# Kernel tuning notes

Measured on AMD Instinct MI355X. Metric: run time of the kernel, lower is better.

The kernel has to match this reference:

```python
import jax, jax.numpy as jnp
import numpy as np

N = 100000   # nodes
D = 8        # in_dim/2 (per-node phase dim)
H = 256      # hidden_dim
E = 1600000  # directed edges (avg degree 16)


def setup_inputs() -> dict:
    key = jax.random.key(0)
    ks = jax.random.split(key, 8)
    q = jax.random.normal(ks[0], (N, D), jnp.float32)
    p = jax.random.normal(ks[1], (N, D), jnp.float32)
    # per-node diagonal positive-definite mass matrix (what get_mass() produces:
    # diag(relu(diag(.)) + 1e-4)); keep it well-conditioned for the inverse.
    m_diag = jax.random.uniform(ks[2], (N, D), jnp.float32) + 0.5
    M = jax.vmap(jnp.diag)(m_diag)  # [N, D, D]
    src = jax.random.randint(ks[3], (E,), 0, N, dtype=jnp.int32)
    off = jax.random.randint(ks[4], (E,), 1, N, dtype=jnp.int32)
    dst = ((src + off) % N).astype(jnp.int32)  # guaranteed no self-edges (euclid>0)
    W1 = jax.random.normal(ks[5], (D, H), jnp.float32) / jnp.sqrt(D)
    b1 = jnp.zeros((H,), jnp.float32)
    W2 = jax.random.normal(ks[6], (H, D), jnp.float32) / jnp.sqrt(H)
    b2 = jnp.zeros((D,), jnp.float32)
    gravity = jnp.ones((1, 1), jnp.float32)
    return {"q": q, "p": p, "M": M, "src": src, "dst": dst,
            "W1": W1, "b1": b1, "W2": W2, "b2": b2, "gravity": gravity}


def _gcn(x, src, dst, norm_src, norm_dst, W, b, n_nodes):
    # DGL GraphConv norm='both': D_out^{-1/2} on src, sum-aggregate, D_in^{-1/2} on dst
    m = (x * norm_src[:, None])[src]                       # [E, F]
    agg = jax.ops.segment_sum(m, dst, num_segments=n_nodes)
    return (agg * norm_dst[:, None]) @ W + b


def reference(q, p, M, src, dst, W1, b1, W2, b2, gravity):
    n = q.shape[0]
    ones_e = jnp.ones(src.shape[0], q.dtype)
    out_deg = jax.ops.segment_sum(ones_e, src, num_segments=n)
    in_deg = jax.ops.segment_sum(ones_e, dst, num_segments=n)
    norm_src = jnp.where(out_deg > 0, out_deg, 1.0) ** -0.5
    norm_dst = jnp.where(in_deg > 0, in_deg, 1.0) ** -0.5

    def P_scalar(qq):
        # ConvGNN: GraphConv -> ReLU -> GraphConv, residual add
        h = jax.nn.relu(_gcn(qq, src, dst, norm_src, norm_dst, W1, b1, n))
        h = _gcn(h, src, dst, norm_src, norm_dst, W2, b2, n) + qq      # [N, D]
        euclid = jnp.linalg.norm(h[src] - h[dst], axis=-1)             # [E]
        masses = M[src] * M[dst]                                       # [E, D, D]
        return 0.5 * jnp.sum(gravity[0, 0] * masses / euclid[:, None, None])

    # dHdq = grad of potential P w.r.t q (torch.autograd.grad in original)
    dHdQ = jax.grad(P_scalar)(q)
    # dHdp: per-node p_i @ inv(M_i)  (self-loop graph, degree 1 per node)
    dHdP = jnp.linalg.solve(jnp.swapaxes(M, -1, -2), p[..., None])[..., 0]
    return jnp.concatenate([dHdQ, dHdP], axis=-1)  # [N, 2D]
```

## Files before the change

kernel.cpp:

```cpp
#include <hip/hip_runtime.h>
#include <hip/hip_fp16.h>

#define DD 8
#define HH 256
#define CH 8192
#define PAYBITS 17
#define PAYMASK 0x1FFFF
#define WPITCH 20


__global__ void k_coarse(const int* __restrict__ src, const int* __restrict__ dst,
                         int* __restrict__ gHistIn, int* __restrict__ gHistOut,
                         int NB, int E) {
    __shared__ int hIn[256], hOut[256];
    if (threadIdx.x < 256) { hIn[threadIdx.x] = 0; hOut[threadIdx.x] = 0; }
    __syncthreads();
    int lo = blockIdx.x * CH;
    int hi = min(lo + CH, E);
    for (int i = lo + threadIdx.x; i < hi; i += blockDim.x) {
        atomicAdd(&hIn[dst[i] >> 9], 1);
        atomicAdd(&hOut[src[i] >> 9], 1);
    }
    __syncthreads();
    if (threadIdx.x < NB) {
        int ci = hIn[threadIdx.x], co = hOut[threadIdx.x];
        if (ci) atomicAdd(&gHistIn[threadIdx.x], ci);
        if (co) atomicAdd(&gHistOut[threadIdx.x], co);
    }
}

__global__ void k_cscan(const int* __restrict__ gHistIn, const int* __restrict__ gHistOut,
                        int* __restrict__ cStartIn, int* __restrict__ cStartOut,
                        int* __restrict__ cCurIn, int* __restrict__ cCurOut,
                        int NB, int E) {
    __shared__ int s[256];
#pragma unroll
    for (int dir = 0; dir < 2; dir++) {
        const int* gh = dir ? gHistOut : gHistIn;
        int* cs = dir ? cStartOut : cStartIn;
        int* cc = dir ? cCurOut : cCurIn;
        int v = (threadIdx.x < NB) ? gh[threadIdx.x] : 0;
        s[threadIdx.x] = v;
        __syncthreads();
        for (int off = 1; off < 256; off <<= 1) {
            int t = (threadIdx.x >= off) ? s[threadIdx.x - off] : 0;
            __syncthreads();
            s[threadIdx.x] += t;
            __syncthreads();
        }
        if (threadIdx.x < NB) {
            int ex = s[threadIdx.x] - v;
            cs[threadIdx.x] = ex;
            cc[threadIdx.x] = ex;
        }
        if (threadIdx.x == 0) cs[NB] = E;
        __syncthreads();
    }
}

__global__ void k_part2(const int* __restrict__ src, const int* __restrict__ dst,
                        int* __restrict__ cCurIn, int* __restrict__ cCurOut,
                        int* __restrict__ P_in, int* __restrict__ P_out,
                        int NB, int E) {
    int dir = blockIdx.y;
    const int* key = dir ? src : dst;
    const int* pay = dir ? dst : src;
    int* cCur = dir ? cCurOut : cCurIn;
    int* P    = dir ? P_out   : P_in;
    __shared__ int h[256];
    if (threadIdx.x < 256) h[threadIdx.x] = 0;
    __syncthreads();
    int lo = blockIdx.x * CH;
    int hi = min(lo + CH, E);
    for (int i = lo + threadIdx.x; i < hi; i += blockDim.x)
        atomicAdd(&h[key[i] >> 9], 1);
    __syncthreads();
    if (threadIdx.x < NB) {
        int c = h[threadIdx.x];
        h[threadIdx.x] = c ? atomicAdd(&cCur[threadIdx.x], c) : 0;
    }
    __syncthreads();
    for (int i = lo + threadIdx.x; i < hi; i += blockDim.x) {
        int k = key[i];
        int pos = atomicAdd(&h[k >> 9], 1);
        P[pos] = ((k & 511) << PAYBITS) | pay[i];
    }
}

__launch_bounds__(512)
__global__ void k_fine2(const int* __restrict__ cStartIn, const int* __restrict__ cStartOut,
                        const int* __restrict__ P_in, const int* __restrict__ P_out,
                        int* __restrict__ start_in, int* __restrict__ start_out,
                        int* __restrict__ csr_in, int* __restrict__ csr_out, int N) {
    int dir = blockIdx.y;
    const int* cStart = dir ? cStartOut : cStartIn;
    const int* P      = dir ? P_out     : P_in;
    int* start        = dir ? start_out : start_in;
    int* csr          = dir ? csr_out   : csr_in;
    __shared__ int cnt[512], scn[512];
    int b = blockIdx.x;
    int lo = cStart[b], hi = cStart[b + 1];
    cnt[threadIdx.x] = 0;
    __syncthreads();
    for (int i = lo + threadIdx.x; i < hi; i += 512)
        atomicAdd(&cnt[P[i] >> PAYBITS], 1);
    __syncthreads();
    int own = cnt[threadIdx.x];
    scn[threadIdx.x] = own;
    __syncthreads();
    for (int off = 1; off < 512; off <<= 1) {
        int t = (threadIdx.x >= off) ? scn[threadIdx.x - off] : 0;
        __syncthreads();
        scn[threadIdx.x] += t;
        __syncthreads();
    }
    int base = lo + scn[threadIdx.x] - own;
    int node = (b << 9) + threadIdx.x;
    if (node < N) start[node] = base;
    cnt[threadIdx.x] = base;
    __syncthreads();
    for (int i = lo + threadIdx.x; i < hi; i += 512) {
        int p = P[i];
        int pos = atomicAdd(&cnt[p >> PAYBITS], 1);
        csr[pos] = p & PAYMASK;
    }
}

__global__ void k_prep(const float* __restrict__ q, const float* __restrict__ p,
                       const float* __restrict__ M,
                       const float* __restrict__ W1, const float* __restrict__ W2,
                       float* __restrict__ W12p,
                       int* __restrict__ start_in, int* __restrict__ start_out,
                       float* __restrict__ a, float* __restrict__ b,
                       __half2* __restrict__ hm, float* __restrict__ qn,
                       float* __restrict__ out, int N, int E) {
    int t = blockIdx.x * blockDim.x + threadIdx.x;
    if (t == 0) { start_in[N] = E; start_out[N] = E; }
    if (t < HH * DD) {
        int j = t >> 3, dd = t & 7;
        W12p[j * WPITCH + dd]     = W1[dd * HH + j];
        W12p[j * WPITCH + 8 + dd] = W2[j * DD + dd];
    }
    int v = t;
    if (v >= N) return;
    int ei1 = (v + 1 < N) ? start_in[v + 1]  : E;
    int eo1 = (v + 1 < N) ? start_out[v + 1] : E;
    float din  = (float)(ei1 - start_in[v]);
    float dout = (float)(eo1 - start_out[v]);
    float av = 1.0f / sqrtf(dout > 0.f ? dout : 1.f);
    float bv = 1.0f / sqrtf(din  > 0.f ? din  : 1.f);
    a[v] = av; b[v] = bv;
#pragma unroll
    for (int d = 0; d < DD; d++) {
        float m = M[(size_t)v * DD * DD + d * (DD + 1)];
        __half2 hmv;
        hmv.x = __float2half(0.f);
        hmv.y = __float2half(m);
        hm[(size_t)v * DD + d] = hmv;
        qn[(size_t)v * DD + d] = av * q[(size_t)v * DD + d];
        out[(size_t)v * 2 * DD + DD + d] = p[(size_t)v * DD + d] / m;
    }
}

static __device__ __forceinline__
float gather_sum(const int* __restrict__ csr, const float* __restrict__ x,
                 int lo, int hi, int d) {
    float s = 0.f;
    int e = lo;
    for (; e + 7 < hi; e += 8) {
        int u[8];
#pragma unroll
        for (int i = 0; i < 8; i++) u[i] = csr[e + i];
        float xv[8];
#pragma unroll
        for (int i = 0; i < 8; i++) xv[i] = x[(size_t)u[i] * DD + d];
        s += ((xv[0] + xv[1]) + (xv[2] + xv[3])) + ((xv[4] + xv[5]) + (xv[6] + xv[7]));
    }
    for (; e + 3 < hi; e += 4) {
        int u0 = csr[e], u1 = csr[e + 1], u2 = csr[e + 2], u3 = csr[e + 3];
        s += (x[(size_t)u0 * DD + d] + x[(size_t)u1 * DD + d])
           + (x[(size_t)u2 * DD + d] + x[(size_t)u3 * DD + d]);
    }
    for (; e < hi; e++) s += x[(size_t)csr[e] * DD + d];
    return s;
}

static __device__ __forceinline__
float gather_sum_h(const int* __restrict__ csr, const __half* __restrict__ x,
                   int lo, int hi, int d) {
    float s = 0.f;
    int e = lo;
    for (; e + 7 < hi; e += 8) {
        int u[8];
#pragma unroll
        for (int i = 0; i < 8; i++) u[i] = csr[e + i];
        float xv[8];
#pragma unroll
        for (int i = 0; i < 8; i++) xv[i] = __half2float(x[(size_t)u[i] * DD + d]);
        s += ((xv[0] + xv[1]) + (xv[2] + xv[3])) + ((xv[4] + xv[5]) + (xv[6] + xv[7]));
    }
    for (; e + 3 < hi; e += 4) {
        int u0 = csr[e], u1 = csr[e + 1], u2 = csr[e + 2], u3 = csr[e + 3];
        s += (__half2float(x[(size_t)u0 * DD + d]) + __half2float(x[(size_t)u1 * DD + d]))
           + (__half2float(x[(size_t)u2 * DD + d]) + __half2float(x[(size_t)u3 * DD + d]));
    }
    for (; e < hi; e++) s += __half2float(x[(size_t)csr[e] * DD + d]);
    return s;
}

__launch_bounds__(256)
__global__ void k_fwd(const int* __restrict__ start, const int* __restrict__ csr,
                      const float* __restrict__ qn, const float* __restrict__ a,
                      const float* __restrict__ b,
                      const float* __restrict__ W12p, const float* __restrict__ b1,
                      float* __restrict__ agg1, float* __restrict__ ya, int N) {
    __shared__ float sW[HH * WPITCH];
    __shared__ float sb1[HH];
    for (int i = threadIdx.x; i < HH * WPITCH; i += 256) sW[i] = W12p[i];
    for (int i = threadIdx.x; i < HH; i += 256) sb1[i] = b1[i];
    __syncthreads();
    int t = blockIdx.x * 256 + threadIdx.x;
    int v = t >> 4, l16 = t & 15, sub = (t >> 3) & 1, d = t & 7;
    if (v >= N) return;
    int e0 = start[v], e1 = start[v + 1];
    int mid = e0 + ((e1 - e0) >> 1);
    float s = gather_sum(csr, qn, sub ? mid : e0, sub ? e1 : mid, d);
    s += __shfl_xor(s, 8);
    if (!sub) agg1[(size_t)v * DD + d] = s;
    float zl = b[v] * s;
    float z[DD];
#pragma unroll
    for (int k = 0; k < DD; k++) z[k] = __shfl(zl, k, 16);
    float acc[DD] = {0.f, 0.f, 0.f, 0.f, 0.f, 0.f, 0.f, 0.f};
    for (int c = 0; c < HH / 16; c += 2) {
        int j0 = (c << 4) | l16, j1 = j0 + 16;
        const float4* w0 = (const float4*)(sW + j0 * WPITCH);
        const float4* w1 = (const float4*)(sW + j1 * WPITCH);
        float4 wa0 = w0[0], wb0 = w0[1], va0 = w0[2], vb0 = w0[3];
        float4 wa1 = w1[0], wb1 = w1[1], va1 = w1[2], vb1 = w1[3];
        float ua0 = fmaf(z[1], wa0.y, fmaf(z[0], wa0.x, sb1[j0]));
        ua0 = fmaf(z[3], wa0.w, fmaf(z[2], wa0.z, ua0));
        float ub0 = fmaf(z[5], wb0.y, z[4] * wb0.x);
        ub0 = fmaf(z[7], wb0.w, fmaf(z[6], wb0.z, ub0));
        float ua1 = fmaf(z[1], wa1.y, fmaf(z[0], wa1.x, sb1[j1]));
        ua1 = fmaf(z[3], wa1.w, fmaf(z[2], wa1.z, ua1));
        float ub1 = fmaf(z[5], wb1.y, z[4] * wb1.x);
        ub1 = fmaf(z[7], wb1.w, fmaf(z[6], wb1.z, ub1));
        float h0 = fmaxf(ua0 + ub0, 0.f);
        float h1 = fmaxf(ua1 + ub1, 0.f);
        acc[0] = fmaf(h0, va0.x, acc[0]); acc[1] = fmaf(h0, va0.y, acc[1]);
        acc[2] = fmaf(h0, va0.z, acc[2]); acc[3] = fmaf(h0, va0.w, acc[3]);
        acc[4] = fmaf(h0, vb0.x, acc[4]); acc[5] = fmaf(h0, vb0.y, acc[5]);
        acc[6] = fmaf(h0, vb0.z, acc[6]); acc[7] = fmaf(h0, vb0.w, acc[7]);
        acc[0] = fmaf(h1, va1.x, acc[0]); acc[1] = fmaf(h1, va1.y, acc[1]);
        acc[2] = fmaf(h1, va1.z, acc[2]); acc[3] = fmaf(h1, va1.w, acc[3]);
        acc[4] = fmaf(h1, vb1.x, acc[4]); acc[5] = fmaf(h1, vb1.y, acc[5]);
        acc[6] = fmaf(h1, vb1.z, acc[6]); acc[7] = fmaf(h1, vb1.w, acc[7]);
    }
#pragma unroll
    for (int m = 1; m < 16; m <<= 1)
#pragma unroll
        for (int k = 0; k < DD; k++) acc[k] += __shfl_xor(acc[k], m);
    float yl = acc[0];
#pragma unroll
    for (int k = 1; k < DD; k++) yl = (d == k) ? acc[k] : yl;
    if (!sub) ya[(size_t)v * DD + d] = a[v] * yl;
}

__global__ void k_h_agg16(const int* __restrict__ start, const int* __restrict__ csr,
                          const float* __restrict__ ya, const float* __restrict__ b,
                          const float* __restrict__ q, const float* __restrict__ b2,
                          __half2* __restrict__ hm, int N) {
    int t = blockIdx.x * blockDim.x + threadIdx.x;
    int v = t >> 4, sub = (t >> 3) & 1, d = t & 7;
    if (v >= N) return;
    int e0 = start[v], e1 = start[v + 1];
    int mid = e0 + ((e1 - e0) >> 1);
    float s = gather_sum(csr, ya, sub ? mid : e0, sub ? e1 : mid, d);
    s += __shfl_xor(s, 8);
    if (!sub) {
        float hval = fmaf(b[v], s, b2[d] + q[(size_t)v * DD + d]);
        ((__half*)hm)[((size_t)v * DD + d) * 2] = __float2half(hval);
    }
}

__global__ void k_gh16(const int* __restrict__ start_in, const int* __restrict__ csr_in,
                       const int* __restrict__ start_out, const int* __restrict__ csr_out,
                       const __half2* __restrict__ hm,
                       const float* __restrict__ b, const float* __restrict__ grav,
                       float* __restrict__ gh, __half* __restrict__ bgh, int N) {
    int t = blockIdx.x * blockDim.x + threadIdx.x;
    int v = t >> 4, dir = (t >> 3) & 1, d = t & 7;
    if (v >= N) return;
    __half2 self = hm[(size_t)v * DD + d];
    float hv = __low2float(self), mv = __high2float(self);
    float coef = -0.5f * grav[0];
    float acc = 0.f;
    const int* start = dir ? start_out : start_in;
    const int* csr   = dir ? csr_out   : csr_in;
    int e1 = start[v + 1];
    int e = start[v];
    for (; e + 3 < e1; e += 4) {
        int u0 = csr[e], u1 = csr[e + 1], u2 = csr[e + 2], u3 = csr[e + 3];
        __half2 q0 = hm[(size_t)u0 * DD + d];
        __half2 q1 = hm[(size_t)u1 * DD + d];
        __half2 q2 = hm[(size_t)u2 * DD + d];
        __half2 q3 = hm[(size_t)u3 * DD + d];
        float d0 = hv - __low2float(q0), d1 = hv - __low2float(q1);
        float d2 = hv - __low2float(q2), d3 = hv - __low2float(q3);
        float e20 = d0 * d0, e21 = d1 * d1, e22 = d2 * d2, e23 = d3 * d3;
        float S0 = mv * __high2float(q0), S1 = mv * __high2float(q1);
        float S2 = mv * __high2float(q2), S3 = mv * __high2float(q3);
        e20 += __shfl_xor(e20, 1); S0 += __shfl_xor(S0, 1);
        e21 += __shfl_xor(e21, 1); S1 += __shfl_xor(S1, 1);
        e22 += __shfl_xor(e22, 1); S2 += __shfl_xor(S2, 1);
        e23 += __shfl_xor(e23, 1); S3 += __shfl_xor(S3, 1);
        e20 += __shfl_xor(e20, 2); S0 += __shfl_xor(S0, 2);
        e21 += __shfl_xor(e21, 2); S1 += __shfl_xor(S1, 2);
        e22 += __shfl_xor(e22, 2); S2 += __shfl_xor(S2, 2);
        e23 += __shfl_xor(e23, 2); S3 += __shfl_xor(S3, 2);
        e20 += __shfl_xor(e20, 4); S0 += __shfl_xor(S0, 4);
        e21 += __shfl_xor(e21, 4); S1 += __shfl_xor(S1, 4);
        e22 += __shfl_xor(e22, 4); S2 += __shfl_xor(S2, 4);
        e23 += __shfl_xor(e23, 4); S3 += __shfl_xor(S3, 4);
        float r0 = rsqrtf(e20), r1 = rsqrtf(e21), r2 = rsqrtf(e22), r3 = rsqrtf(e23);
        float c0 = coef * S0 * r0 * r0 * r0;
        float c1 = coef * S1 * r1 * r1 * r1;
        float c2 = coef * S2 * r2 * r2 * r2;
        float c3 = coef * S3 * r3 * r3 * r3;
        acc = fmaf(c0, d0, acc); acc = fmaf(c1, d1, acc);
        acc = fmaf(c2, d2, acc); acc = fmaf(c3, d3, acc);
    }
    for (; e < e1; e++) {
        int u = csr[e];
        __half2 qu = hm[(size_t)u * DD + d];
        float dif = hv - __low2float(qu);
        float e2 = dif * dif;
        float S  = mv * __high2float(qu);
        e2 += __shfl_xor(e2, 1); S += __shfl_xor(S, 1);
        e2 += __shfl_xor(e2, 2); S += __shfl_xor(S, 2);
        e2 += __shfl_xor(e2, 4); S += __shfl_xor(S, 4);
        float r = rsqrtf(e2);
        acc = fmaf(coef * S * r * r * r, dif, acc);
    }
    acc += __shfl_xor(acc, 8);
    if (!dir) {
        gh[(size_t)v * DD + d] = acc;
        bgh[(size_t)v * DD + d] = __float2half(b[v] * acc);
    }
}

__launch_bounds__(256)
__global__ void k_bwd(const int* __restrict__ start, const int* __restrict__ csr,
                      const __half* __restrict__ bgh, const float* __restrict__ agg1,
                      const float* __restrict__ a, const float* __restrict__ b,
                      const float* __restrict__ W12p, const float* __restrict__ b1,
                      __half* __restrict__ gz1b, int N) {
    __shared__ float sW[HH * WPITCH];
    __shared__ float sb1[HH];
    for (int i = threadIdx.x; i < HH * WPITCH; i += 256) sW[i] = W12p[i];
    for (int i = threadIdx.x; i < HH; i += 256) sb1[i] = b1[i];
    __syncthreads();
    int t = blockIdx.x * 256 + threadIdx.x;
    int v = t >> 4, l16 = t & 15, sub = (t >> 3) & 1, d = t & 7;
    if (v >= N) return;
    int e0 = start[v], e1 = start[v + 1];
    int mid = e0 + ((e1 - e0) >> 1);
    float s = gather_sum_h(csr, bgh, sub ? mid : e0, sub ? e1 : mid, d);
    s += __shfl_xor(s, 8);
    float bv = b[v], av = a[v];
    float zl = bv * agg1[(size_t)v * DD + d];
    float z[DD], gq[DD];
#pragma unroll
    for (int k = 0; k < DD; k++) { z[k] = __shfl(zl, k, 16); gq[k] = __shfl(s, k, 16); }
    float gz[DD] = {0.f, 0.f, 0.f, 0.f, 0.f, 0.f, 0.f, 0.f};
    for (int c = 0; c < HH / 16; c += 2) {
        int j0 = (c << 4) | l16, j1 = j0 + 16;
        const float4* w0 = (const float4*)(sW + j0 * WPITCH);
        const float4* w1 = (const float4*)(sW + j1 * WPITCH);
        float4 wa0 = w0[0], wb0 = w0[1], va0 = w0[2], vb0 = w0[3];
        float4 wa1 = w1[0], wb1 = w1[1], va1 = w1[2], vb1 = w1[3];
        float ua0 = fmaf(z[1], wa0.y, fmaf(z[0], wa0.x, sb1[j0]));
        ua0 = fmaf(z[3], wa0.w, fmaf(z[2], wa0.z, ua0));
        float ub0 = fmaf(z[5], wb0.y, z[4] * wb0.x);
        ub0 = fmaf(z[7], wb0.w, fmaf(z[6], wb0.z, ub0));
        float ua1 = fmaf(z[1], wa1.y, fmaf(z[0], wa1.x, sb1[j1]));
        ua1 = fmaf(z[3], wa1.w, fmaf(z[2], wa1.z, ua1));
        float ub1 = fmaf(z[5], wb1.y, z[4] * wb1.x);
        ub1 = fmaf(z[7], wb1.w, fmaf(z[6], wb1.z, ub1));
        float u0 = ua0 + ub0, u1 = ua1 + ub1;
        float ga0 = fmaf(gq[1], va0.y, gq[0] * va0.x);
        ga0 = fmaf(gq[3], va0.w, fmaf(gq[2], va0.z, ga0));
        float gb0 = fmaf(gq[5], vb0.y, gq[4] * vb0.x);
        gb0 = fmaf(gq[7], vb0.w, fmaf(gq[6], vb0.z, gb0));
        float ga1 = fmaf(gq[1], va1.y, gq[0] * va1.x);
        ga1 = fmaf(gq[3], va1.w, fmaf(gq[2], va1.z, ga1));
        float gb1 = fmaf(gq[5], vb1.y, gq[4] * vb1.x);
        gb1 = fmaf(gq[7], vb1.w, fmaf(gq[6], vb1.z, gb1));
        float g0 = (u0 > 0.f) ? av * (ga0 + gb0) : 0.f;
        float g1 = (u1 > 0.f) ? av * (ga1 + gb1) : 0.f;
        gz[0] = fmaf(g0, wa0.x, gz[0]); gz[1] = fmaf(g0, wa0.y, gz[1]);
        gz[2] = fmaf(g0, wa0.z, gz[2]); gz[3] = fmaf(g0, wa0.w, gz[3]);
        gz[4] = fmaf(g0, wb0.x, gz[4]); gz[5] = fmaf(g0, wb0.y, gz[5]);
        gz[6] = fmaf(g0, wb0.z, gz[6]); gz[7] = fmaf(g0, wb0.w, gz[7]);
        gz[0] = fmaf(g1, wa1.x, gz[0]); gz[1] = fmaf(g1, wa1.y, gz[1]);
        gz[2] = fmaf(g1, wa1.z, gz[2]); gz[3] = fmaf(g1, wa1.w, gz[3]);
        gz[4] = fmaf(g1, wb1.x, gz[4]); gz[5] = fmaf(g1, wb1.y, gz[5]);
        gz[6] = fmaf(g1, wb1.z, gz[6]); gz[7] = fmaf(g1, wb1.w, gz[7]);
    }
#pragma unroll
    for (int m = 1; m < 16; m <<= 1)
#pragma unroll
        for (int k = 0; k < DD; k++) gz[k] += __shfl_xor(gz[k], m);
    float out_l = gz[0];
#pragma unroll
    for (int k = 1; k < DD; k++) out_l = (d == k) ? gz[k] : out_l;
    if (!sub) gz1b[(size_t)v * DD + d] = __float2half(bv * out_l);
}

__global__ void k_out_agg16(const int* __restrict__ start, const int* __restrict__ csr,
                            const __half* __restrict__ gz1b, const float* __restrict__ gh,
                            const float* __restrict__ a, float* __restrict__ out, int N) {
    int t = blockIdx.x * blockDim.x + threadIdx.x;
    int v = t >> 4, sub = (t >> 3) & 1, d = t & 7;
    if (v >= N) return;
    int e0 = start[v], e1 = start[v + 1];
    int mid = e0 + ((e1 - e0) >> 1);
    float s = gather_sum_h(csr, gz1b, sub ? mid : e0, sub ? e1 : mid, d);
    s += __shfl_xor(s, 8);
    if (!sub)
        out[(size_t)v * 2 * DD + d] = fmaf(a[v], s, gh[(size_t)v * DD + d]);
}


extern "C" void kernel_launch(void* const* d_in, const int* in_sizes, int n_in,
                              void* d_out, int out_size, void* d_ws, size_t ws_size,
                              hipStream_t stream) {
    const float* q    = (const float*)d_in[0];
    const float* p    = (const float*)d_in[1];
    const float* M    = (const float*)d_in[2];
    const int*   src  = (const int*)d_in[3];
    const int*   dst  = (const int*)d_in[4];
    const float* W1   = (const float*)d_in[5];
    const float* b1   = (const float*)d_in[6];
    const float* W2   = (const float*)d_in[7];
    const float* b2   = (const float*)d_in[8];
    const float* grav = (const float*)d_in[9];
    float* out = (float*)d_out;

    int N = in_sizes[0] / DD;
    int E = in_sizes[3];
    size_t n = (size_t)N;
    int NB = (N + 511) >> 9;

    float*   ws   = (float*)d_ws;
    float*   a_   = ws;
    float*   b_   = ws + n;
    float*   qn   = ws + 2  * n;
    float*   agg1 = ws + 10 * n;
    float*   ya   = ws + 18 * n;
    float*   gh   = ws + 26 * n;
    __half2* hm   = (__half2*)(ws + 34 * n);
    __half*  bgh  = (__half*)(ws + 42 * n);
    __half*  gz1b = (__half*)(ws + 46 * n);

    int* iw        = (int*)(ws + 50 * n);
    int* csr_in    = iw;
    int* csr_out   = iw + (size_t)E;
    int* start_in  = iw + 2 * (size_t)E;
    int* start_out = start_in + n + 1;
    int* gHistIn   = start_out + n + 1;
    int* gHistOut  = gHistIn + 256;
    int* cStartIn  = gHistOut + 256;
    int* cStartOut = cStartIn + NB + 1;
    int* cCurIn    = cStartOut + NB + 1;
    int* cCurOut   = cCurIn + NB;
    int* iwEnd     = cCurOut + NB;
    float* W12p    = (float*)iwEnd;
    int* intAfter  = (int*)(W12p + HH * WPITCH);
    int* P_in  = (E <= 16 * (long long)n) ? (int*)ws            : intAfter;
    int* P_out = (E <= 16 * (long long)n) ? (int*)(ws + 16 * n) : intAfter + E;

    hipMemsetAsync(gHistIn, 0, 512 * sizeof(int), stream);

    const int tb = 256;
    int gbN  = (N + tb - 1) / tb;
    int gb16 = (int)((16 * n + tb - 1) / tb);
    int gbC  = (E + CH - 1) / CH;

    k_coarse <<<gbC, tb, 0, stream>>>(src, dst, gHistIn, gHistOut, NB, E);
    k_cscan  <<<1, 256, 0, stream>>>(gHistIn, gHistOut, cStartIn, cStartOut,
                                     cCurIn, cCurOut, NB, E);
    k_part2  <<<dim3(gbC, 2), tb, 0, stream>>>(src, dst, cCurIn, cCurOut,
                                               P_in, P_out, NB, E);
    k_fine2  <<<dim3(NB, 2), 512, 0, stream>>>(cStartIn, cStartOut, P_in, P_out,
                                               start_in, start_out, csr_in, csr_out, N);
    k_prep   <<<gbN, tb, 0, stream>>>(q, p, M, W1, W2, W12p, start_in, start_out,
                                      a_, b_, hm, qn, out, N, E);

    k_fwd    <<<gb16, tb, 0, stream>>>(start_in, csr_in, qn, a_, b_,
                                       W12p, b1, agg1, ya, N);
    k_h_agg16<<<gb16, tb, 0, stream>>>(start_in, csr_in, ya, b_, q, b2, hm, N);
    k_gh16   <<<gb16, tb, 0, stream>>>(start_in, csr_in, start_out, csr_out,
                                       hm, b_, grav, gh, bgh, N);
    k_bwd    <<<gb16, tb, 0, stream>>>(start_out, csr_out, bgh, agg1, a_, b_,
                                       W12p, b1, gz1b, N);
    k_out_agg16<<<gb16, tb, 0, stream>>>(start_out, csr_out, gz1b, gh, a_, out, N);
}
```

Measured before the change: 354.7 us.

## Split gathers into per-node-thread vector-load kernels separate from MLP kernels

```diff
diff --git a/kernel.cpp b/kernel.cpp
--- a/kernel.cpp
+++ b/kernel.cpp
@@ -163,57 +163,210 @@
 }
 
 static __device__ __forceinline__
-float gather_sum(const int* __restrict__ csr, const float* __restrict__ x,
-                 int lo, int hi, int d) {
-    float s = 0.f;
-    int e = lo;
-    for (; e + 7 < hi; e += 8) {
-        int u[8];
-#pragma unroll
-        for (int i = 0; i < 8; i++) u[i] = csr[e + i];
-        float xv[8];
-#pragma unroll
-        for (int i = 0; i < 8; i++) xv[i] = x[(size_t)u[i] * DD + d];
-        s += ((xv[0] + xv[1]) + (xv[2] + xv[3])) + ((xv[4] + xv[5]) + (xv[6] + xv[7]));
-    }
-    for (; e + 3 < hi; e += 4) {
+void acc_h8(uint4 r, float acc[8]) {
+    float2 f;
+    f = __half22float2(*(__half2*)&r.x); acc[0] += f.x; acc[1] += f.y;
+    f = __half22float2(*(__half2*)&r.y); acc[2] += f.x; acc[3] += f.y;
+    f = __half22float2(*(__half2*)&r.z); acc[4] += f.x; acc[5] += f.y;
+    f = __half22float2(*(__half2*)&r.w); acc[6] += f.x; acc[7] += f.y;
+}
+
+static __device__ __forceinline__
+void unpack_hm(uint4 r0, uint4 r1, float h[8], float m[8]) {
+    float2 f;
+    f = __half22float2(*(__half2*)&r0.x); h[0] = f.x; m[0] = f.y;
+    f = __half22float2(*(__half2*)&r0.y); h[1] = f.x; m[1] = f.y;
+    f = __half22float2(*(__half2*)&r0.z); h[2] = f.x; m[2] = f.y;
+    f = __half22float2(*(__half2*)&r0.w); h[3] = f.x; m[3] = f.y;
+    f = __half22float2(*(__half2*)&r1.x); h[4] = f.x; m[4] = f.y;
+    f = __half22float2(*(__half2*)&r1.y); h[5] = f.x; m[5] = f.y;
+    f = __half22float2(*(__half2*)&r1.z); h[6] = f.x; m[6] = f.y;
+    f = __half22float2(*(__half2*)&r1.w); h[7] = f.x; m[7] = f.y;
+}
+
+static __device__ __forceinline__
+void gather_h8(const int* __restrict__ csr, const __half* __restrict__ x,
+               int e, int e1, float acc[8]) {
+    for (; e + 3 < e1; e += 4) {
         int u0 = csr[e], u1 = csr[e + 1], u2 = csr[e + 2], u3 = csr[e + 3];
-        s += (x[(size_t)u0 * DD + d] + x[(size_t)u1 * DD + d])
-           + (x[(size_t)u2 * DD + d] + x[(size_t)u3 * DD + d]);
-    }
-    for (; e < hi; e++) s += x[(size_t)csr[e] * DD + d];
-    return s;
-}
-
-static __device__ __forceinline__
-float gather_sum_h(const int* __restrict__ csr, const __half* __restrict__ x,
-                   int lo, int hi, int d) {
-    float s = 0.f;
-    int e = lo;
-    for (; e + 7 < hi; e += 8) {
-        int u[8];
-#pragma unroll
-        for (int i = 0; i < 8; i++) u[i] = csr[e + i];
-        float xv[8];
-#pragma unroll
-        for (int i = 0; i < 8; i++) xv[i] = __half2float(x[(size_t)u[i] * DD + d]);
-        s += ((xv[0] + xv[1]) + (xv[2] + xv[3])) + ((xv[4] + xv[5]) + (xv[6] + xv[7]));
-    }
-    for (; e + 3 < hi; e += 4) {
-        int u0 = csr[e], u1 = csr[e + 1], u2 = csr[e + 2], u3 = csr[e + 3];
-        s += (__half2float(x[(size_t)u0 * DD + d]) + __half2float(x[(size_t)u1 * DD + d]))
-           + (__half2float(x[(size_t)u2 * DD + d]) + __half2float(x[(size_t)u3 * DD + d]));
-    }
-    for (; e < hi; e++) s += __half2float(x[(size_t)csr[e] * DD + d]);
-    return s;
-}
+        uint4 r0 = *(const uint4*)(x + (size_t)u0 * DD);
+        uint4 r1 = *(const uint4*)(x + (size_t)u1 * DD);
+        uint4 r2 = *(const uint4*)(x + (size_t)u2 * DD);
+        uint4 r3 = *(const uint4*)(x + (size_t)u3 * DD);
+        acc_h8(r0, acc); acc_h8(r1, acc); acc_h8(r2, acc); acc_h8(r3, acc);
+    }
+    for (; e < e1; e++) {
+        uint4 r = *(const uint4*)(x + (size_t)csr[e] * DD);
+        acc_h8(r, acc);
+    }
+}
+
+
+__launch_bounds__(64)
+__global__ void k_agg_node(const int* __restrict__ start, const int* __restrict__ csr,
+                           const float* __restrict__ x, float* __restrict__ y, int N) {
+    int v = blockIdx.x * 64 + threadIdx.x;
+    if (v >= N) return;
+    int e = start[v], e1 = start[v + 1];
+    float acc[8] = {0.f, 0.f, 0.f, 0.f, 0.f, 0.f, 0.f, 0.f};
+    for (; e + 1 < e1; e += 2) {
+        int u0 = csr[e], u1 = csr[e + 1];
+        const float4* p0 = (const float4*)(x + (size_t)u0 * DD);
+        const float4* p1 = (const float4*)(x + (size_t)u1 * DD);
+        float4 a0 = p0[0], b0 = p0[1], a1 = p1[0], b1 = p1[1];
+        acc[0] += a0.x + a1.x; acc[1] += a0.y + a1.y;
+        acc[2] += a0.z + a1.z; acc[3] += a0.w + a1.w;
+        acc[4] += b0.x + b1.x; acc[5] += b0.y + b1.y;
+        acc[6] += b0.z + b1.z; acc[7] += b0.w + b1.w;
+    }
+    if (e < e1) {
+        const float4* p = (const float4*)(x + (size_t)csr[e] * DD);
+        float4 a0 = p[0], b0 = p[1];
+        acc[0] += a0.x; acc[1] += a0.y; acc[2] += a0.z; acc[3] += a0.w;
+        acc[4] += b0.x; acc[5] += b0.y; acc[6] += b0.z; acc[7] += b0.w;
+    }
+    float4* yp = (float4*)(y + (size_t)v * DD);
+    yp[0] = make_float4(acc[0], acc[1], acc[2], acc[3]);
+    yp[1] = make_float4(acc[4], acc[5], acc[6], acc[7]);
+}
+
+__launch_bounds__(64)
+__global__ void k_h_node(const int* __restrict__ start, const int* __restrict__ csr,
+                         const __half* __restrict__ ya, const float* __restrict__ b,
+                         const float* __restrict__ q, const float* __restrict__ b2,
+                         __half2* __restrict__ hm, int N) {
+    int v = blockIdx.x * 64 + threadIdx.x;
+    if (v >= N) return;
+    float acc[8] = {0.f, 0.f, 0.f, 0.f, 0.f, 0.f, 0.f, 0.f};
+    gather_h8(csr, ya, start[v], start[v + 1], acc);
+    float bv = b[v];
+    const float4* qp = (const float4*)(q + (size_t)v * DD);
+    float4 q0 = qp[0], q1 = qp[1];
+    float hq[8] = {q0.x, q0.y, q0.z, q0.w, q1.x, q1.y, q1.z, q1.w};
+    __half2* hp = hm + (size_t)v * DD;
+#pragma unroll
+    for (int k = 0; k < DD; k++) {
+        float hval = fmaf(bv, acc[k], b2[k] + hq[k]);
+        __half2 cur = hp[k];
+        cur.x = __float2half(hval);
+        hp[k] = cur;
+    }
+}
+
+__launch_bounds__(64)
+__global__ void k_gh2(const int* __restrict__ start_in, const int* __restrict__ csr_in,
+                      const int* __restrict__ start_out, const int* __restrict__ csr_out,
+                      const __half2* __restrict__ hm,
+                      const float* __restrict__ b, const float* __restrict__ grav,
+                      float* __restrict__ gh, __half* __restrict__ bgh, int N) {
+    int t = blockIdx.x * 64 + threadIdx.x;
+    int v = t >> 1, dir = t & 1;
+    if (v >= N) return;
+    const uint4* srec = (const uint4*)(hm + (size_t)v * DD);
+    uint4 s0 = srec[0], s1 = srec[1];
+    float hv[8], mv[8];
+    unpack_hm(s0, s1, hv, mv);
+    const int* start = dir ? start_out : start_in;
+    const int* csr   = dir ? csr_out   : csr_in;
+    int e = start[v], e1 = start[v + 1];
+    float coef = -0.5f * grav[0];
+    float acc[8] = {0.f, 0.f, 0.f, 0.f, 0.f, 0.f, 0.f, 0.f};
+    for (; e + 1 < e1; e += 2) {
+        int u0 = csr[e], u1 = csr[e + 1];
+        const uint4* r0p = (const uint4*)(hm + (size_t)u0 * DD);
+        const uint4* r1p = (const uint4*)(hm + (size_t)u1 * DD);
+        uint4 x0 = r0p[0], x1 = r0p[1], y0 = r1p[0], y1 = r1p[1];
+        float hu0[8], mu0[8], hu1[8], mu1[8];
+        unpack_hm(x0, x1, hu0, mu0);
+        unpack_hm(y0, y1, hu1, mu1);
+        float d0[8], d1[8];
+        float e20 = 0.f, S0 = 0.f, e21 = 0.f, S1 = 0.f;
+#pragma unroll
+        for (int k = 0; k < 8; k++) {
+            d0[k] = hv[k] - hu0[k];
+            d1[k] = hv[k] - hu1[k];
+            e20 = fmaf(d0[k], d0[k], e20);
+            e21 = fmaf(d1[k], d1[k], e21);
+            S0 = fmaf(mv[k], mu0[k], S0);
+            S1 = fmaf(mv[k], mu1[k], S1);
+        }
+        float r0 = rsqrtf(e20), r1 = rsqrtf(e21);
+        float c0 = coef * S0 * r0 * r0 * r0;
+        float c1 = coef * S1 * r1 * r1 * r1;
+#pragma unroll
+        for (int k = 0; k < 8; k++)
+            acc[k] = fmaf(c0, d0[k], fmaf(c1, d1[k], acc[k]));
+    }
+    if (e < e1) {
+        int u = csr[e];
+        const uint4* rp = (const uint4*)(hm + (size_t)u * DD);
+        uint4 x0 = rp[0], x1 = rp[1];
+        float hu[8], mu[8];
+        unpack_hm(x0, x1, hu, mu);
+        float df[8];
+        float e2 = 0.f, S = 0.f;
+#pragma unroll
+        for (int k = 0; k < 8; k++) {
+            df[k] = hv[k] - hu[k];
+            e2 = fmaf(df[k], df[k], e2);
+            S = fmaf(mv[k], mu[k], S);
+        }
+        float r = rsqrtf(e2);
+        float c = coef * S * r * r * r;
+#pragma unroll
+        for (int k = 0; k < 8; k++) acc[k] = fmaf(c, df[k], acc[k]);
+    }
+#pragma unroll
+    for (int k = 0; k < 8; k++) acc[k] += __shfl_xor(acc[k], 1);
+    if (!dir) {
+        float4* gp = (float4*)(gh + (size_t)v * DD);
+        gp[0] = make_float4(acc[0], acc[1], acc[2], acc[3]);
+        gp[1] = make_float4(acc[4], acc[5], acc[6], acc[7]);
+        float bv = b[v];
+        __half2* bp = (__half2*)(bgh + (size_t)v * DD);
+        bp[0] = __floats2half2_rn(bv * acc[0], bv * acc[1]);
+        bp[1] = __floats2half2_rn(bv * acc[2], bv * acc[3]);
+        bp[2] = __floats2half2_rn(bv * acc[4], bv * acc[5]);
+        bp[3] = __floats2half2_rn(bv * acc[6], bv * acc[7]);
+    }
+}
+
+__launch_bounds__(64)
+__global__ void k_bgh_node(const int* __restrict__ start, const int* __restrict__ csr,
+                           const __half* __restrict__ bgh, float* __restrict__ gq2, int N) {
+    int v = blockIdx.x * 64 + threadIdx.x;
+    if (v >= N) return;
+    float acc[8] = {0.f, 0.f, 0.f, 0.f, 0.f, 0.f, 0.f, 0.f};
+    gather_h8(csr, bgh, start[v], start[v + 1], acc);
+    float4* yp = (float4*)(gq2 + (size_t)v * DD);
+    yp[0] = make_float4(acc[0], acc[1], acc[2], acc[3]);
+    yp[1] = make_float4(acc[4], acc[5], acc[6], acc[7]);
+}
+
+__launch_bounds__(64)
+__global__ void k_out_node(const int* __restrict__ start, const int* __restrict__ csr,
+                           const __half* __restrict__ gz1b, const float* __restrict__ gh,
+                           const float* __restrict__ a, float* __restrict__ out, int N) {
+    int v = blockIdx.x * 64 + threadIdx.x;
+    if (v >= N) return;
+    float acc[8] = {0.f, 0.f, 0.f, 0.f, 0.f, 0.f, 0.f, 0.f};
+    gather_h8(csr, gz1b, start[v], start[v + 1], acc);
+    float av = a[v];
+    const float4* gp = (const float4*)(gh + (size_t)v * DD);
+    float4 g0 = gp[0], g1 = gp[1];
+    float4* op = (float4*)(out + (size_t)v * 2 * DD);
+    op[0] = make_float4(fmaf(av, acc[0], g0.x), fmaf(av, acc[1], g0.y),
+                        fmaf(av, acc[2], g0.z), fmaf(av, acc[3], g0.w));
+    op[1] = make_float4(fmaf(av, acc[4], g1.x), fmaf(av, acc[5], g1.y),
+                        fmaf(av, acc[6], g1.z), fmaf(av, acc[7], g1.w));
+}
+
 
 __launch_bounds__(256)
-__global__ void k_fwd(const int* __restrict__ start, const int* __restrict__ csr,
-                      const float* __restrict__ qn, const float* __restrict__ a,
-                      const float* __restrict__ b,
-                      const float* __restrict__ W12p, const float* __restrict__ b1,
-                      float* __restrict__ agg1, float* __restrict__ ya, int N) {
+__global__ void k_mlp_fwd(const float* __restrict__ agg1, const float* __restrict__ a,
+                          const float* __restrict__ b,
+                          const float* __restrict__ W12p, const float* __restrict__ b1,
+                          __half* __restrict__ ya, int N) {
     __shared__ float sW[HH * WPITCH];
     __shared__ float sb1[HH];
     for (int i = threadIdx.x; i < HH * WPITCH; i += 256) sW[i] = W12p[i];
@@ -222,12 +375,7 @@
     int t = blockIdx.x * 256 + threadIdx.x;
     int v = t >> 4, l16 = t & 15, sub = (t >> 3) & 1, d = t & 7;
     if (v >= N) return;
-    int e0 = start[v], e1 = start[v + 1];
-    int mid = e0 + ((e1 - e0) >> 1);
-    float s = gather_sum(csr, qn, sub ? mid : e0, sub ? e1 : mid, d);
-    s += __shfl_xor(s, 8);
-    if (!sub) agg1[(size_t)v * DD + d] = s;
-    float zl = b[v] * s;
+    float zl = b[v] * agg1[(size_t)v * DD + d];
     float z[DD];
 #pragma unroll
     for (int k = 0; k < DD; k++) z[k] = __shfl(zl, k, 16);
@@ -264,98 +412,14 @@
     float yl = acc[0];
 #pragma unroll
     for (int k = 1; k < DD; k++) yl = (d == k) ? acc[k] : yl;
-    if (!sub) ya[(size_t)v * DD + d] = a[v] * yl;
-}
-
-__global__ void k_h_agg16(const int* __restrict__ start, const int* __restrict__ csr,
-                          const float* __restrict__ ya, const float* __restrict__ b,
-                          const float* __restrict__ q, const float* __restrict__ b2,
-                          __half2* __restrict__ hm, int N) {
-    int t = blockIdx.x * blockDim.x + threadIdx.x;
-    int v = t >> 4, sub = (t >> 3) & 1, d = t & 7;
-    if (v >= N) return;
-    int e0 = start[v], e1 = start[v + 1];
-    int mid = e0 + ((e1 - e0) >> 1);
-    float s = gather_sum(csr, ya, sub ? mid : e0, sub ? e1 : mid, d);
-    s += __shfl_xor(s, 8);
-    if (!sub) {
-        float hval = fmaf(b[v], s, b2[d] + q[(size_t)v * DD + d]);
-        ((__half*)hm)[((size_t)v * DD + d) * 2] = __float2half(hval);
-    }
-}
-
-__global__ void k_gh16(const int* __restrict__ start_in, const int* __restrict__ csr_in,
-                       const int* __restrict__ start_out, const int* __restrict__ csr_out,
-                       const __half2* __restrict__ hm,
-                       const float* __restrict__ b, const float* __restrict__ grav,
-                       float* __restrict__ gh, __half* __restrict__ bgh, int N) {
-    int t = blockIdx.x * blockDim.x + threadIdx.x;
-    int v = t >> 4, dir = (t >> 3) & 1, d = t & 7;
-    if (v >= N) return;
-    __half2 self = hm[(size_t)v * DD + d];
-    float hv = __low2float(self), mv = __high2float(self);
-    float coef = -0.5f * grav[0];
-    float acc = 0.f;
-    const int* start = dir ? start_out : start_in;
-    const int* csr   = dir ? csr_out   : csr_in;
-    int e1 = start[v + 1];
-    int e = start[v];
-    for (; e + 3 < e1; e += 4) {
-        int u0 = csr[e], u1 = csr[e + 1], u2 = csr[e + 2], u3 = csr[e + 3];
-        __half2 q0 = hm[(size_t)u0 * DD + d];
-        __half2 q1 = hm[(size_t)u1 * DD + d];
-        __half2 q2 = hm[(size_t)u2 * DD + d];
-        __half2 q3 = hm[(size_t)u3 * DD + d];
-        float d0 = hv - __low2float(q0), d1 = hv - __low2float(q1);
-        float d2 = hv - __low2float(q2), d3 = hv - __low2float(q3);
-        float e20 = d0 * d0, e21 = d1 * d1, e22 = d2 * d2, e23 = d3 * d3;
-        float S0 = mv * __high2float(q0), S1 = mv * __high2float(q1);
-        float S2 = mv * __high2float(q2), S3 = mv * __high2float(q3);
-        e20 += __shfl_xor(e20, 1); S0 += __shfl_xor(S0, 1);
-        e21 += __shfl_xor(e21, 1); S1 += __shfl_xor(S1, 1);
-        e22 += __shfl_xor(e22, 1); S2 += __shfl_xor(S2, 1);
-        e23 += __shfl_xor(e23, 1); S3 += __shfl_xor(S3, 1);
-        e20 += __shfl_xor(e20, 2); S0 += __shfl_xor(S0, 2);
-        e21 += __shfl_xor(e21, 2); S1 += __shfl_xor(S1, 2);
-        e22 += __shfl_xor(e22, 2); S2 += __shfl_xor(S2, 2);
-        e23 += __shfl_xor(e23, 2); S3 += __shfl_xor(S3, 2);
-        e20 += __shfl_xor(e20, 4); S0 += __shfl_xor(S0, 4);
-        e21 += __shfl_xor(e21, 4); S1 += __shfl_xor(S1, 4);
-        e22 += __shfl_xor(e22, 4); S2 += __shfl_xor(S2, 4);
-        e23 += __shfl_xor(e23, 4); S3 += __shfl_xor(S3, 4);
-        float r0 = rsqrtf(e20), r1 = rsqrtf(e21), r2 = rsqrtf(e22), r3 = rsqrtf(e23);
-        float c0 = coef * S0 * r0 * r0 * r0;
-        float c1 = coef * S1 * r1 * r1 * r1;
-        float c2 = coef * S2 * r2 * r2 * r2;
-        float c3 = coef * S3 * r3 * r3 * r3;
-        acc = fmaf(c0, d0, acc); acc = fmaf(c1, d1, acc);
-        acc = fmaf(c2, d2, acc); acc = fmaf(c3, d3, acc);
-    }
-    for (; e < e1; e++) {
-        int u = csr[e];
-        __half2 qu = hm[(size_t)u * DD + d];
-        float dif = hv - __low2float(qu);
-        float e2 = dif * dif;
-        float S  = mv * __high2float(qu);
-        e2 += __shfl_xor(e2, 1); S += __shfl_xor(S, 1);
-        e2 += __shfl_xor(e2, 2); S += __shfl_xor(S, 2);
-        e2 += __shfl_xor(e2, 4); S += __shfl_xor(S, 4);
-        float r = rsqrtf(e2);
-        acc = fmaf(coef * S * r * r * r, dif, acc);
-    }
-    acc += __shfl_xor(acc, 8);
-    if (!dir) {
-        gh[(size_t)v * DD + d] = acc;
-        bgh[(size_t)v * DD + d] = __float2half(b[v] * acc);
-    }
+    if (!sub) ya[(size_t)v * DD + d] = __float2half(a[v] * yl);
 }
 
 __launch_bounds__(256)
-__global__ void k_bwd(const int* __restrict__ start, const int* __restrict__ csr,
-                      const __half* __restrict__ bgh, const float* __restrict__ agg1,
-                      const float* __restrict__ a, const float* __restrict__ b,
-                      const float* __restrict__ W12p, const float* __restrict__ b1,
-                      __half* __restrict__ gz1b, int N) {
+__global__ void k_mlp_bwd(const float* __restrict__ gq2, const float* __restrict__ agg1,
+                          const float* __restrict__ a, const float* __restrict__ b,
+                          const float* __restrict__ W12p, const float* __restrict__ b1,
+                          __half* __restrict__ gz1b, int N) {
     __shared__ float sW[HH * WPITCH];
     __shared__ float sb1[HH];
     for (int i = threadIdx.x; i < HH * WPITCH; i += 256) sW[i] = W12p[i];
@@ -364,15 +428,12 @@
     int t = blockIdx.x * 256 + threadIdx.x;
     int v = t >> 4, l16 = t & 15, sub = (t >> 3) & 1, d = t & 7;
     if (v >= N) return;
-    int e0 = start[v], e1 = start[v + 1];
-    int mid = e0 + ((e1 - e0) >> 1);
-    float s = gather_sum_h(csr, bgh, sub ? mid : e0, sub ? e1 : mid, d);
-    s += __shfl_xor(s, 8);
     float bv = b[v], av = a[v];
     float zl = bv * agg1[(size_t)v * DD + d];
+    float gl = gq2[(size_t)v * DD + d];
     float z[DD], gq[DD];
 #pragma unroll
-    for (int k = 0; k < DD; k++) { z[k] = __shfl(zl, k, 16); gq[k] = __shfl(s, k, 16); }
+    for (int k = 0; k < DD; k++) { z[k] = __shfl(zl, k, 16); gq[k] = __shfl(gl, k, 16); }
     float gz[DD] = {0.f, 0.f, 0.f, 0.f, 0.f, 0.f, 0.f, 0.f};
     for (int c = 0; c < HH / 16; c += 2) {
         int j0 = (c << 4) | l16, j1 = j0 + 16;
@@ -418,20 +479,6 @@
     if (!sub) gz1b[(size_t)v * DD + d] = __float2half(bv * out_l);
 }
 
-__global__ void k_out_agg16(const int* __restrict__ start, const int* __restrict__ csr,
-                            const __half* __restrict__ gz1b, const float* __restrict__ gh,
-                            const float* __restrict__ a, float* __restrict__ out, int N) {
-    int t = blockIdx.x * blockDim.x + threadIdx.x;
-    int v = t >> 4, sub = (t >> 3) & 1, d = t & 7;
-    if (v >= N) return;
-    int e0 = start[v], e1 = start[v + 1];
-    int mid = e0 + ((e1 - e0) >> 1);
-    float s = gather_sum_h(csr, gz1b, sub ? mid : e0, sub ? e1 : mid, d);
-    s += __shfl_xor(s, 8);
-    if (!sub)
-        out[(size_t)v * 2 * DD + d] = fmaf(a[v], s, gh[(size_t)v * DD + d]);
-}
-
 
 extern "C" void kernel_launch(void* const* d_in, const int* in_sizes, int n_in,
                               void* d_out, int out_size, void* d_ws, size_t ws_size,
@@ -458,13 +505,14 @@
     float*   b_   = ws + n;
     float*   qn   = ws + 2  * n;
     float*   agg1 = ws + 10 * n;
-    float*   ya   = ws + 18 * n;
-    float*   gh   = ws + 26 * n;
-    __half2* hm   = (__half2*)(ws + 34 * n);
-    __half*  bgh  = (__half*)(ws + 42 * n);
-    __half*  gz1b = (__half*)(ws + 46 * n);
-
-    int* iw        = (int*)(ws + 50 * n);
+    float*   gh   = ws + 18 * n;
+    __half2* hm   = (__half2*)(ws + 26 * n);
+    __half*  ya   = (__half*)(ws + 34 * n);
+    __half*  bgh  = (__half*)(ws + 38 * n);
+    __half*  gz1b = (__half*)(ws + 42 * n);
+    float*   gq2  = qn;
+
+    int* iw        = (int*)(ws + 46 * n);
     int* csr_in    = iw;
     int* csr_out   = iw + (size_t)E;
     int* start_in  = iw + 2 * (size_t)E;
@@ -485,25 +533,27 @@
 
     const int tb = 256;
     int gbN  = (N + tb - 1) / tb;
+    int gb1  = (N + 63) / 64;
+    int gb2  = (2 * N + 63) / 64;
     int gb16 = (int)((16 * n + tb - 1) / tb);
     int gbC  = (E + CH - 1) / CH;
 
-    k_coarse <<<gbC, tb, 0, stream>>>(src, dst, gHistIn, gHistOut, NB, E);
-    k_cscan  <<<1, 256, 0, stream>>>(gHistIn, gHistOut, cStartIn, cStartOut,
-                                     cCurIn, cCurOut, NB, E);
-    k_part2  <<<dim3(gbC, 2), tb, 0, stream>>>(src, dst, cCurIn, cCurOut,
-                                               P_in, P_out, NB, E);
-    k_fine2  <<<dim3(NB, 2), 512, 0, stream>>>(cStartIn, cStartOut, P_in, P_out,
-                                               start_in, start_out, csr_in, csr_out, N);
-    k_prep   <<<gbN, tb, 0, stream>>>(q, p, M, W1, W2, W12p, start_in, start_out,
-                                      a_, b_, hm, qn, out, N, E);
-
-    k_fwd    <<<gb16, tb, 0, stream>>>(start_in, csr_in, qn, a_, b_,
-                                       W12p, b1, agg1, ya, N);
-    k_h_agg16<<<gb16, tb, 0, stream>>>(start_in, csr_in, ya, b_, q, b2, hm, N);
-    k_gh16   <<<gb16, tb, 0, stream>>>(start_in, csr_in, start_out, csr_out,
+    k_coarse  <<<gbC, tb, 0, stream>>>(src, dst, gHistIn, gHistOut, NB, E);
+    k_cscan   <<<1, 256, 0, stream>>>(gHistIn, gHistOut, cStartIn, cStartOut,
+                                      cCurIn, cCurOut, NB, E);
+    k_part2   <<<dim3(gbC, 2), tb, 0, stream>>>(src, dst, cCurIn, cCurOut,
+                                                P_in, P_out, NB, E);
+    k_fine2   <<<dim3(NB, 2), 512, 0, stream>>>(cStartIn, cStartOut, P_in, P_out,
+                                                start_in, start_out, csr_in, csr_out, N);
+    k_prep    <<<gbN, tb, 0, stream>>>(q, p, M, W1, W2, W12p, start_in, start_out,
+                                       a_, b_, hm, qn, out, N, E);
+
+    k_agg_node<<<gb1, 64, 0, stream>>>(start_in, csr_in, qn, agg1, N);
+    k_mlp_fwd <<<gb16, tb, 0, stream>>>(agg1, a_, b_, W12p, b1, ya, N);
+    k_h_node  <<<gb1, 64, 0, stream>>>(start_in, csr_in, ya, b_, q, b2, hm, N);
+    k_gh2     <<<gb2, 64, 0, stream>>>(start_in, csr_in, start_out, csr_out,
                                        hm, b_, grav, gh, bgh, N);
-    k_bwd    <<<gb16, tb, 0, stream>>>(start_out, csr_out, bgh, agg1, a_, b_,
-                                       W12p, b1, gz1b, N);
-    k_out_agg16<<<gb16, tb, 0, stream>>>(start_out, csr_out, gz1b, gh, a_, out, N);
-}
+    k_bgh_node<<<gb1, 64, 0, stream>>>(start_out, csr_out, bgh, gq2, N);
+    k_mlp_bwd <<<gb16, tb, 0, stream>>>(gq2, agg1, a_, b_, W12p, b1, gz1b, N);
+    k_out_node<<<gb1, 64, 0, stream>>>(start_out, csr_out, gz1b, gh, a_, out, N);
+}
```

New measurement: 350.1 us. No clear change (-1.3%).
